# Optimization experiments

Measured on AMD Instinct MI355X. Metric: run time of the kernel, lower is better.

## Reference

```python
import jax, jax.numpy as jnp
import numpy as np

B, T, C, H = 2, 2048, 2048, 16
HD = C // H  # head dim = 128
BASE = 10000.0


def _rope_tables(seq_len, d):
    p = jnp.arange(d // 2, dtype=jnp.float32)
    # faithful to source: exponent uses 2**p (power of two), not 2*p
    theta = jnp.power(BASE, -(2.0 ** p) / d)            # [d/2]
    pos = jnp.arange(1, seq_len + 1, dtype=jnp.float32)[:, None]  # 1-indexed positions
    c = pos * theta                                      # [T, d/2]
    ang = jnp.concatenate([c, c], axis=-1)               # [T, d]
    return jnp.cos(ang), jnp.sin(ang)


def _rope(x):
    # x: [B, H, T, d]
    d = x.shape[-1]
    cos, sin = _rope_tables(x.shape[-2], d)
    half = d // 2
    x_rot = jnp.concatenate([-x[..., half:], x[..., :half]], axis=-1)
    return x * cos + x_rot * sin


def setup_inputs() -> dict:
    key = jax.random.key(0)
    k1, k2, k3 = jax.random.split(key, 3)
    x = jax.random.normal(k1, (B, T, C), dtype=jnp.float32)
    Wqkv = jax.random.normal(k2, (3 * C, C), dtype=jnp.float32) * 0.02
    bqkv = jnp.zeros((3 * C,), dtype=jnp.float32)
    Wo = jax.random.normal(k3, (C, C), dtype=jnp.float32) * 0.02
    bo = jnp.zeros((C,), dtype=jnp.float32)
    return {"x": x, "Wqkv": Wqkv, "bqkv": bqkv, "Wo": Wo, "bo": bo}


def reference(x, Wqkv, bqkv, Wo, bo):
    b, t, c = x.shape
    qkv = x @ Wqkv.T + bqkv                      # [B, T, 3C]
    q, k, v = jnp.split(qkv, 3, axis=-1)
    # [B, T, C] -> [B, H, T, HD]
    def to_heads(z):
        return z.reshape(b, t, H, HD).transpose(0, 2, 1, 3)
    q, k, v = to_heads(q), to_heads(k), to_heads(v)
    q = _rope(q)
    k = _rope(k)
    scale = 1.0 / jnp.sqrt(jnp.float32(HD))
    att = jnp.einsum('bhqd,bhkd->bhqk', q, k) * scale   # [B, H, T, T]
    causal = jnp.tril(jnp.ones((t, t), dtype=bool))
    att = jnp.where(causal, att, -jnp.inf)
    att = jax.nn.softmax(att, axis=-1)
    y = jnp.einsum('bhqk,bhkd->bhqd', att, v)           # [B, H, T, HD]
    y = y.transpose(0, 2, 1, 3).reshape(b, t, c)
    y = y @ Wo.T + bo
    return y
```

## Files before the change

kernel.cpp:

```cpp
#include <hip/hip_runtime.h>
#include <hip/hip_bf16.h>


typedef __attribute__((ext_vector_type(8))) short short8;
typedef __attribute__((ext_vector_type(4))) float f32x4;

#define B_  2
#define T_  2048
#define C_  2048
#define H_  16
#define HD_ 128

#define BARRIER() asm volatile("s_barrier" ::: "memory")
#define LGKM0()   asm volatile("s_waitcnt lgkmcnt(0)" ::: "memory")

template<int N> __device__ __forceinline__ void vmwait() {
  if constexpr (N == 8)      asm volatile("s_waitcnt vmcnt(8)" ::: "memory");
  else if constexpr (N == 6) asm volatile("s_waitcnt vmcnt(6)" ::: "memory");
  else if constexpr (N == 4) asm volatile("s_waitcnt vmcnt(4)" ::: "memory");
  else if constexpr (N == 3) asm volatile("s_waitcnt vmcnt(3)" ::: "memory");
  else if constexpr (N == 0) asm volatile("s_waitcnt vmcnt(0)" ::: "memory");
}

__device__ __forceinline__ float bf2f(unsigned short u) {
  union { unsigned int i; float f; } v; v.i = ((unsigned int)u) << 16; return v.f;
}
__device__ __forceinline__ unsigned short f2bf(float f) {
  union { float f; unsigned int i; } v; v.f = f;
  unsigned int x = v.i;
  return (unsigned short)((x + 0x7fffu + ((x >> 16) & 1u)) >> 16);
}
__device__ __forceinline__ float fexp2(float x) {
#if __has_builtin(__builtin_amdgcn_exp2f)
  return __builtin_amdgcn_exp2f(x);
#else
  return exp2f(x);
#endif
}

__device__ __forceinline__ void gll16(const unsigned short* g, unsigned short* lds_base) {
  __builtin_amdgcn_global_load_lds(
      (const __attribute__((address_space(1))) void*)g,
      (__attribute__((address_space(3))) void*)lds_base, 16, 0, 0);
}

__global__ void cvt_k(const float* __restrict__ src, unsigned short* __restrict__ dst, int n4)
{
  int i = blockIdx.x * blockDim.x + threadIdx.x;
  if (i < n4) {
    float4 v = ((const float4*)src)[i];
    ushort4 h;
    h.x = f2bf(v.x); h.y = f2bf(v.y); h.z = f2bf(v.z); h.w = f2bf(v.w);
    ((ushort4*)dst)[i] = h;
  }
}

__device__ __forceinline__ void stage_unit(
    const unsigned short* __restrict__ G, int K, int t, int kk,
    unsigned short (&L)[2][2][2][256][32], int buf, int mat,
    int wave, int sra, int ca8)
{
  const unsigned short* s = G + (size_t)sra * K + t * 64 + kk * 32 + ca8;
  gll16(s,                   &L[buf][kk][mat][wave * 16][0]);
  gll16(s + (size_t)128 * K, &L[buf][kk][mat][128 + wave * 16][0]);
}

template<int CB, bool SN1, bool SN2, int V0, int V1, int V2, int V3>
__device__ __forceinline__ void ktile256(
    int t,
    const unsigned short* __restrict__ Ag,
    const unsigned short* __restrict__ Bg, int K,
    unsigned short (&L)[2][2][2][256][32],
    f32x4 (&acc)[8][4],
    int wave, int wm, int wn, int l15, int csw8, int sra, int ca8)
{
  short8 af[4], bf[4];

#pragma unroll
  for (int n = 0; n < 4; ++n)
    bf[n] = *(const short8*)&L[CB][0][1][wn * 64 + n * 16 + l15][csw8];
#pragma unroll
  for (int j = 0; j < 4; ++j)
    af[j] = *(const short8*)&L[CB][0][0][wm * 128 + j * 16 + l15][csw8];
  if constexpr (SN1)
    stage_unit(Ag, K, t + 1, 1, L, CB ^ 1, 0, wave, sra, ca8);
  BARRIER();
  LGKM0();
  __builtin_amdgcn_s_setprio(1);
#pragma unroll
  for (int j = 0; j < 4; ++j)
#pragma unroll
    for (int n = 0; n < 4; ++n)
      acc[j][n] = __builtin_amdgcn_mfma_f32_16x16x32_bf16(af[j], bf[n], acc[j][n], 0, 0, 0);
  __builtin_amdgcn_s_setprio(0);
  vmwait<V0>();
  BARRIER();

#pragma unroll
  for (int j = 0; j < 4; ++j)
    af[j] = *(const short8*)&L[CB][0][0][wm * 128 + 64 + j * 16 + l15][csw8];
  if constexpr (SN1)
    stage_unit(Bg, K, t + 1, 1, L, CB ^ 1, 1, wave, sra, ca8);
  BARRIER();
  LGKM0();
  __builtin_amdgcn_s_setprio(1);
#pragma unroll
  for (int j = 0; j < 4; ++j)
#pragma unroll
    for (int n = 0; n < 4; ++n)
      acc[4 + j][n] = __builtin_amdgcn_mfma_f32_16x16x32_bf16(af[j], bf[n], acc[4 + j][n], 0, 0, 0);
  __builtin_amdgcn_s_setprio(0);
  vmwait<V1>();
  BARRIER();

#pragma unroll
  for (int n = 0; n < 4; ++n)
    bf[n] = *(const short8*)&L[CB][1][1][wn * 64 + n * 16 + l15][csw8];
#pragma unroll
  for (int j = 0; j < 4; ++j)
    af[j] = *(const short8*)&L[CB][1][0][wm * 128 + j * 16 + l15][csw8];
  if constexpr (SN2)
    stage_unit(Ag, K, t + 2, 0, L, CB, 0, wave, sra, ca8);
  BARRIER();
  LGKM0();
  __builtin_amdgcn_s_setprio(1);
#pragma unroll
  for (int j = 0; j < 4; ++j)
#pragma unroll
    for (int n = 0; n < 4; ++n)
      acc[j][n] = __builtin_amdgcn_mfma_f32_16x16x32_bf16(af[j], bf[n], acc[j][n], 0, 0, 0);
  __builtin_amdgcn_s_setprio(0);
  vmwait<V2>();
  BARRIER();

#pragma unroll
  for (int j = 0; j < 4; ++j)
    af[j] = *(const short8*)&L[CB][1][0][wm * 128 + 64 + j * 16 + l15][csw8];
  if constexpr (SN2)
    stage_unit(Bg, K, t + 2, 0, L, CB, 1, wave, sra, ca8);
  BARRIER();
  LGKM0();
  __builtin_amdgcn_s_setprio(1);
#pragma unroll
  for (int j = 0; j < 4; ++j)
#pragma unroll
    for (int n = 0; n < 4; ++n)
      acc[4 + j][n] = __builtin_amdgcn_mfma_f32_16x16x32_bf16(af[j], bf[n], acc[4 + j][n], 0, 0, 0);
  __builtin_amdgcn_s_setprio(0);
  vmwait<V3>();
  BARRIER();
}

template<int MODE>
__global__ __launch_bounds__(512, 2)
void gemm256(const unsigned short* __restrict__ A,
             const unsigned short* __restrict__ Bw,
             const float* __restrict__ bias,
             float* __restrict__ Cout,
             unsigned short* __restrict__ Qb,
             unsigned short* __restrict__ Kb,
             unsigned short* __restrict__ Vb,
             int N, int K)
{
  __shared__ unsigned short L[2][2][2][256][32];

  const int tid  = threadIdx.x;
  const int wave = tid >> 6, lane = tid & 63;
  const int quad = lane >> 4, l15 = lane & 15;
  const int wm = wave >> 2, wn = wave & 3;
  const int csw8 = (quad ^ ((l15 >> 1) & 3)) * 8;
  const int sra = tid >> 2;
  const int ca8 = ((tid & 3) ^ ((sra >> 1) & 3)) * 8;

  const int n0 = blockIdx.x * 256;
  const int m0 = blockIdx.y * 256;
  const unsigned short* Ag = A  + (size_t)m0 * K;
  const unsigned short* Bg = Bw + (size_t)n0 * K;

  f32x4 acc[8][4];
#pragma unroll
  for (int i = 0; i < 8; i++)
#pragma unroll
    for (int j = 0; j < 4; j++) acc[i][j] = (f32x4){0.f, 0.f, 0.f, 0.f};

  stage_unit(Ag, K, 0, 0, L, 0, 0, wave, sra, ca8);
  stage_unit(Bg, K, 0, 0, L, 0, 1, wave, sra, ca8);
  stage_unit(Ag, K, 0, 1, L, 0, 0, wave, sra, ca8);
  stage_unit(Bg, K, 0, 1, L, 0, 1, wave, sra, ca8);
  stage_unit(Ag, K, 1, 0, L, 1, 0, wave, sra, ca8);
  stage_unit(Bg, K, 1, 0, L, 1, 1, wave, sra, ca8);
  vmwait<8>();
  BARRIER();

  const int NT = K >> 6;
#pragma unroll 1
  for (int t = 0; t + 3 < NT; t += 2) {
    ktile256<0, true, true, 8, 8, 8, 8>(t,     Ag, Bg, K, L, acc, wave, wm, wn, l15, csw8, sra, ca8);
    ktile256<1, true, true, 8, 8, 8, 8>(t + 1, Ag, Bg, K, L, acc, wave, wm, wn, l15, csw8, sra, ca8);
  }
  ktile256<0, true,  false, 8,  8,  8,  4>(NT - 2, Ag, Bg, K, L, acc, wave, wm, wn, l15, csw8, sra, ca8);
  ktile256<1, false, false, -1, 0, -1, -1>(NT - 1, Ag, Bg, K, L, acc, wave, wm, wn, l15, csw8, sra, ca8);

  if constexpr (MODE == 0) {
#pragma unroll
    for (int mi = 0; mi < 8; mi++)
#pragma unroll
      for (int n = 0; n < 4; n++) {
        int col = n0 + wn * 64 + n * 16 + l15;
        float bv = bias[col];
#pragma unroll
        for (int r = 0; r < 4; r++) {
          int row = m0 + wm * 128 + mi * 16 + quad * 4 + r;
          Cout[(size_t)row * N + col] = acc[mi][n][r] + bv;
        }
      }
  } else {
    const int which = n0 >> 11;
    unsigned short* P = (which == 0) ? Qb : (which == 1) ? Kb : Vb;
#pragma unroll
    for (int mi = 0; mi < 8; mi++)
#pragma unroll
      for (int n = 0; n < 4; n++) {
        int col = n0 + wn * 64 + n * 16 + l15;
        float bv = bias[col];
        int h = (col >> 7) & 15, d = col & 127;
#pragma unroll
        for (int r = 0; r < 4; r++) {
          int m = m0 + wm * 128 + mi * 16 + quad * 4 + r;
          int b = m >> 11, t = m & (T_ - 1);
          size_t addr = (which == 2)
              ? ((size_t)((b * H_ + h) * HD_ + d)) * T_ + t
              : ((size_t)((b * H_ + h) * T_ + t)) * HD_ + d;
          P[addr] = f2bf(acc[mi][n][r] + bv);
        }
      }
  }
}

__global__ void rope_k(unsigned short* __restrict__ Q, unsigned short* __restrict__ K)
{
  const int tid = threadIdx.x;
  const int w = tid >> 6, l = tid & 63;
  const int r = blockIdx.x * 4 + w;
  const int t = r & (T_ - 1);
  const float pos = (float)(t + 1);
  const float theta = expf(-exp2f((float)l) * 0.07195578415606394f);
  const float ang = pos * theta;
  const float c = cosf(ang), s = sinf(ang);
  const float QS = 0.08838834764831845f * 1.4426950408889634f;
  const size_t base = (size_t)r * HD_;

  float q0 = bf2f(Q[base + l]), q1 = bf2f(Q[base + l + 64]);
  Q[base + l]      = f2bf((q0 * c - q1 * s) * QS);
  Q[base + l + 64] = f2bf((q1 * c + q0 * s) * QS);
  float k0 = bf2f(K[base + l]), k1 = bf2f(K[base + l + 64]);
  K[base + l]      = f2bf(k0 * c - k1 * s);
  K[base + l + 64] = f2bf(k1 * c + k0 * s);
}

__global__ __launch_bounds__(256, 2)
void attn_k(const unsigned short* __restrict__ Q,
            const unsigned short* __restrict__ K,
            const unsigned short* __restrict__ Vt_g,
            unsigned short* __restrict__ AO)
{
  __shared__ unsigned short Kl[64 * 128];
  __shared__ unsigned short Vl[128 * 64];
  __shared__ unsigned short Pl[4 * 16 * 72];

  const int tid  = threadIdx.x;
  const int wave = tid >> 6, lane = tid & 63;
  const int quad = lane >> 4, l15 = lane & 15;
  const int blk = blockIdx.x;
  const int bh = (blk & 7) + 8 * ((blk >> 3) & 3);
  const int qp = (blk >> 5) & 15;
  const unsigned short* Qh = Q    + (size_t)bh * T_ * HD_;
  const unsigned short* Kh = K    + (size_t)bh * T_ * HD_;
  const unsigned short* Vh = Vt_g + (size_t)bh * T_ * HD_;
  const int b = bh >> 4, h = bh & 15;

#pragma unroll
  for (int tile = 0; tile < 2; tile++) {
    const int q0 = (tile == 0 ? qp : 31 - qp) * 64;
    const int wq = q0 + wave * 16;
    short8 qf[4];
#pragma unroll
    for (int kc = 0; kc < 4; kc++)
      qf[kc] = *(const short8*)&Qh[(size_t)(wq + l15) * HD_ + kc * 32 + quad * 8];

    f32x4 oacc[8];
#pragma unroll
    for (int n = 0; n < 8; n++) oacc[n] = (f32x4){0.f, 0.f, 0.f, 0.f};
    float mst[4], lst[4];
#pragma unroll
    for (int r = 0; r < 4; r++) { mst[r] = -1e30f; lst[r] = 0.f; }

    const int niter = (q0 >> 6) + 1;
    for (int it = 0; it < niter; it++) {
      const int kt = it * 64;
      __syncthreads();
#pragma unroll
      for (int i = 0; i < 4; i++) {
        int cc = i * 256 + wave * 64 + lane;
        int kr = cc >> 4, kcs = (cc & 15) ^ (kr & 15);
        gll16(Kh + (size_t)(kt + kr) * HD_ + kcs * 8, &Kl[(i * 4 + wave) * 512]);
        int vr = cc >> 3, vcs = (cc & 7) ^ (vr & 7);
        gll16(Vh + (size_t)vr * T_ + kt + vcs * 8, &Vl[(i * 4 + wave) * 512]);
      }
      __syncthreads();

      f32x4 sa[4];
#pragma unroll
      for (int ni = 0; ni < 4; ni++) sa[ni] = (f32x4){0.f, 0.f, 0.f, 0.f};
#pragma unroll
      for (int kc = 0; kc < 4; kc++) {
        const int cswK = (((kc * 4 + quad) ^ l15) * 8);
        short8 bfr[4];
#pragma unroll
        for (int ni = 0; ni < 4; ni++)
          bfr[ni] = *(const short8*)&Kl[(ni * 16 + l15) * HD_ + cswK];
#pragma unroll
        for (int ni = 0; ni < 4; ni++)
          sa[ni] = __builtin_amdgcn_mfma_f32_16x16x32_bf16(qf[kc], bfr[ni], sa[ni], 0, 0, 0);
      }

      if (kt == q0) {
#pragma unroll
        for (int ni = 0; ni < 4; ni++) {
          int gcol = kt + ni * 16 + l15;
#pragma unroll
          for (int r = 0; r < 4; r++) {
            int grow = wq + quad * 4 + r;
            if (gcol > grow) sa[ni][r] = -1e30f;
          }
        }
      }

      float rmax[4] = {-1e30f, -1e30f, -1e30f, -1e30f};
#pragma unroll
      for (int ni = 0; ni < 4; ni++)
#pragma unroll
        for (int r = 0; r < 4; r++) rmax[r] = fmaxf(rmax[r], sa[ni][r]);
#pragma unroll
      for (int r = 0; r < 4; r++)
#pragma unroll
        for (int off = 1; off < 16; off <<= 1)
          rmax[r] = fmaxf(rmax[r], __shfl_xor(rmax[r], off));
      float alpha[4];
#pragma unroll
      for (int r = 0; r < 4; r++) {
        float mnew = fmaxf(mst[r], rmax[r]);
        alpha[r] = fexp2(fminf(mst[r] - mnew, 0.f));
        mst[r] = mnew;
      }
      float rsum[4] = {0.f, 0.f, 0.f, 0.f};
#pragma unroll
      for (int ni = 0; ni < 4; ni++)
#pragma unroll
        for (int r = 0; r < 4; r++) {
          float p = fexp2(fminf(sa[ni][r] - mst[r], 0.f));
          sa[ni][r] = p;
          rsum[r] += p;
        }
#pragma unroll
      for (int r = 0; r < 4; r++) {
#pragma unroll
        for (int off = 1; off < 16; off <<= 1)
          rsum[r] += __shfl_xor(rsum[r], off);
        lst[r] = lst[r] * alpha[r] + rsum[r];
      }
#pragma unroll
      for (int nv = 0; nv < 8; nv++)
#pragma unroll
        for (int r = 0; r < 4; r++) oacc[nv][r] *= alpha[r];
#pragma unroll
      for (int ni = 0; ni < 4; ni++)
#pragma unroll
        for (int r = 0; r < 4; r++)
          Pl[wave * 16 * 72 + (quad * 4 + r) * 72 + ni * 16 + l15] = f2bf(sa[ni][r]);
      __syncthreads();

      short8 pf[2];
#pragma unroll
      for (int kc = 0; kc < 2; kc++)
        pf[kc] = *(const short8*)&Pl[wave * 16 * 72 + l15 * 72 + kc * 32 + quad * 8];
#pragma unroll
      for (int kc = 0; kc < 2; kc++) {
        const int cswV = (((kc * 4 + quad) ^ (l15 & 7)) * 8);
#pragma unroll
        for (int nv = 0; nv < 8; nv++) {
          short8 vb = *(const short8*)&Vl[(nv * 16 + l15) * 64 + cswV];
          oacc[nv] = __builtin_amdgcn_mfma_f32_16x16x32_bf16(pf[kc], vb, oacc[nv], 0, 0, 0);
        }
      }
    }

    float linv[4];
#pragma unroll
    for (int r = 0; r < 4; r++) linv[r] = 1.0f / fmaxf(lst[r], 1e-20f);
#pragma unroll
    for (int nv = 0; nv < 8; nv++)
#pragma unroll
      for (int r = 0; r < 4; r++) {
        int t = wq + quad * 4 + r;
        int d = nv * 16 + l15;
        AO[((size_t)(b * T_ + t)) * C_ + h * HD_ + d] = f2bf(oacc[nv][r] * linv[r]);
      }
  }
}

template<int A32, int B32, int MODE>
__global__ __launch_bounds__(256, 2)
void gemm_nt(const void* __restrict__ Ap, const void* __restrict__ Bp,
             const float* __restrict__ bias,
             float* __restrict__ Cout,
             unsigned short* __restrict__ Qb,
             unsigned short* __restrict__ Kb,
             unsigned short* __restrict__ Vb,
             int N, int K)
{
  __shared__ unsigned short Al[128 * 72];
  __shared__ unsigned short Bl[128 * 72];
  const int tid  = threadIdx.x;
  const int wave = tid >> 6, lane = tid & 63;
  const int quad = lane >> 4, l15 = lane & 15;
  const int wm = wave >> 1, wn = wave & 1;
  const int n0 = blockIdx.x * 128, m0 = blockIdx.y * 128;

  f32x4 acc[4][4];
#pragma unroll
  for (int i = 0; i < 4; i++)
#pragma unroll
    for (int j = 0; j < 4; j++) acc[i][j] = (f32x4){0.f, 0.f, 0.f, 0.f};

  for (int k0 = 0; k0 < K; k0 += 64) {
    __syncthreads();
    if constexpr (A32) {
      const float* A = (const float*)Ap;
#pragma unroll
      for (int i = 0; i < 8; i++) {
        int cid = tid + i * 256;
        int r = cid >> 4, c = cid & 15;
        float4 v = *(const float4*)&A[(size_t)(m0 + r) * K + k0 + c * 4];
        ushort4 hh;
        hh.x = f2bf(v.x); hh.y = f2bf(v.y); hh.z = f2bf(v.z); hh.w = f2bf(v.w);
        *(ushort4*)&Al[r * 72 + c * 4] = hh;
      }
    } else {
      const unsigned short* A = (const unsigned short*)Ap;
#pragma unroll
      for (int i = 0; i < 4; i++) {
        int cid = tid + i * 256;
        int r = cid >> 3, c = cid & 7;
        *(float4*)&Al[r * 72 + c * 8] =
            *(const float4*)&A[(size_t)(m0 + r) * K + k0 + c * 8];
      }
    }
    if constexpr (B32) {
      const float* Bm = (const float*)Bp;
#pragma unroll
      for (int i = 0; i < 8; i++) {
        int cid = tid + i * 256;
        int r = cid >> 4, c = cid & 15;
        float4 v = *(const float4*)&Bm[(size_t)(n0 + r) * K + k0 + c * 4];
        ushort4 hh;
        hh.x = f2bf(v.x); hh.y = f2bf(v.y); hh.z = f2bf(v.z); hh.w = f2bf(v.w);
        *(ushort4*)&Bl[r * 72 + c * 4] = hh;
      }
    } else {
      const unsigned short* Bm = (const unsigned short*)Bp;
#pragma unroll
      for (int i = 0; i < 4; i++) {
        int cid = tid + i * 256;
        int r = cid >> 3, c = cid & 7;
        *(float4*)&Bl[r * 72 + c * 8] =
            *(const float4*)&Bm[(size_t)(n0 + r) * K + k0 + c * 8];
      }
    }
    __syncthreads();
#pragma unroll
    for (int kc = 0; kc < 2; kc++) {
      short8 af[4], bfr[4];
#pragma unroll
      for (int mi = 0; mi < 4; mi++)
        af[mi] = *(const short8*)&Al[(wm * 64 + mi * 16 + l15) * 72 + kc * 32 + quad * 8];
#pragma unroll
      for (int ni = 0; ni < 4; ni++)
        bfr[ni] = *(const short8*)&Bl[(wn * 64 + ni * 16 + l15) * 72 + kc * 32 + quad * 8];
#pragma unroll
      for (int mi = 0; mi < 4; mi++)
#pragma unroll
        for (int ni = 0; ni < 4; ni++)
          acc[mi][ni] = __builtin_amdgcn_mfma_f32_16x16x32_bf16(af[mi], bfr[ni], acc[mi][ni], 0, 0, 0);
    }
  }

  if constexpr (MODE == 0) {
#pragma unroll
    for (int mi = 0; mi < 4; mi++)
#pragma unroll
      for (int ni = 0; ni < 4; ni++) {
        int col = n0 + wn * 64 + ni * 16 + l15;
        float bv = bias[col];
#pragma unroll
        for (int r = 0; r < 4; r++) {
          int row = m0 + wm * 64 + mi * 16 + quad * 4 + r;
          Cout[(size_t)row * N + col] = acc[mi][ni][r] + bv;
        }
      }
  } else {
    int which = n0 >> 11;
    int h = (n0 >> 7) & 15;
    unsigned short* P = (which == 0) ? Qb : (which == 1) ? Kb : Vb;
#pragma unroll
    for (int mi = 0; mi < 4; mi++)
#pragma unroll
      for (int ni = 0; ni < 4; ni++) {
        int d = wn * 64 + ni * 16 + l15;
        float bv = bias[n0 + d];
#pragma unroll
        for (int r = 0; r < 4; r++) {
          int m = m0 + wm * 64 + mi * 16 + quad * 4 + r;
          int b = m >> 11, t = m & (T_ - 1);
          size_t addr = (which == 2)
              ? ((size_t)((b * H_ + h) * HD_ + d)) * T_ + t
              : ((size_t)((b * H_ + h) * T_ + t)) * HD_ + d;
          P[addr] = f2bf(acc[mi][ni][r] + bv);
        }
      }
  }
}

extern "C" void kernel_launch(void* const* d_in, const int* in_sizes, int n_in,
                              void* d_out, int out_size, void* d_ws, size_t ws_size,
                              hipStream_t stream)
{
  const float* x    = (const float*)d_in[0];
  const float* Wqkv = (const float*)d_in[1];
  const float* bqkv = (const float*)d_in[2];
  const float* Wo   = (const float*)d_in[3];
  const float* bo   = (const float*)d_in[4];
  float* out = (float*)d_out;

  const size_t SZ   = (size_t)B_ * H_ * T_ * HD_;
  const size_t NX   = SZ;
  const size_t NWQ  = (size_t)3 * C_ * C_;
  const size_t NWO  = (size_t)C_ * C_;
  unsigned short* ws = (unsigned short*)d_ws;

  dim3 blk(256, 1, 1);
  dim3 blk512(512, 1, 1);
  const size_t need = (NX + NWQ + 3 * SZ) * sizeof(unsigned short);

  if (ws_size >= need) {
    unsigned short* xb    = ws;
    unsigned short* Wqkvb = xb + NX;
    unsigned short* Qb    = Wqkvb + NWQ;
    unsigned short* Kb    = Qb + SZ;
    unsigned short* Vb    = Kb + SZ;
    unsigned short* AO    = xb;
    unsigned short* Wob   = Wqkvb;

    cvt_k<<<dim3((unsigned)(NX / 1024)), blk, 0, stream>>>(x, xb, (int)(NX / 4));
    cvt_k<<<dim3((unsigned)(NWQ / 1024)), blk, 0, stream>>>(Wqkv, Wqkvb, (int)(NWQ / 4));
    gemm256<1><<<dim3(24, 16, 1), blk512, 0, stream>>>(
        xb, Wqkvb, bqkv, nullptr, Qb, Kb, Vb, 6144, 2048);
    cvt_k<<<dim3((unsigned)(NWO / 1024)), blk, 0, stream>>>(Wo, Wob, (int)(NWO / 4));
    rope_k<<<dim3((B_ * H_ * T_) / 4, 1, 1), blk, 0, stream>>>(Qb, Kb);
    attn_k<<<dim3(512, 1, 1), blk, 0, stream>>>(Qb, Kb, Vb, AO);
    gemm256<0><<<dim3(8, 16, 1), blk512, 0, stream>>>(
        AO, Wob, bo, out, nullptr, nullptr, nullptr, 2048, 2048);
  } else {
    unsigned short* Qb = ws;
    unsigned short* Kb = Qb + SZ;
    unsigned short* Vb = Kb + SZ;
    unsigned short* AO = Vb + SZ;
    gemm_nt<1, 1, 1><<<dim3(48, 32, 1), blk, 0, stream>>>(
        (const void*)x, (const void*)Wqkv, bqkv, nullptr, Qb, Kb, Vb, 6144, 2048);
    rope_k<<<dim3((B_ * H_ * T_) / 4, 1, 1), blk, 0, stream>>>(Qb, Kb);
    attn_k<<<dim3(512, 1, 1), blk, 0, stream>>>(Qb, Kb, Vb, AO);
    gemm_nt<0, 1, 0><<<dim3(16, 32, 1), blk, 0, stream>>>(
        (const void*)AO, (const void*)Wo, bo, out, nullptr, nullptr, nullptr, 2048, 2048);
  }
}
```

Measured before the change: 432.4 us.

## Double-buffer GEMM LDS fragments in registers to overlap reads with MFMA

Restructures the 256x256 GEMM k-tile loop so A/B fragments are held in two register sets. Each phase's LDS reads now prefetch operands for a later MFMA phase, including the next tile's first fragments, instead of being read and then waited on with lgkmcnt(0) right before use. The vmcnt waits are rebalanced and two of the four per-tile global-load waits are removed. This aims to hide LDS latency behind MFMA work, at the cost of more live VGPRs and less explicit LDS wait ordering.

```diff
diff --git a/kernel.cpp b/kernel.cpp
--- a/kernel.cpp
+++ b/kernel.cpp
@@ -12,13 +12,11 @@
 #define HD_ 128
 
 #define BARRIER() asm volatile("s_barrier" ::: "memory")
-#define LGKM0()   asm volatile("s_waitcnt lgkmcnt(0)" ::: "memory")
 
 template<int N> __device__ __forceinline__ void vmwait() {
   if constexpr (N == 8)      asm volatile("s_waitcnt vmcnt(8)" ::: "memory");
   else if constexpr (N == 6) asm volatile("s_waitcnt vmcnt(6)" ::: "memory");
   else if constexpr (N == 4) asm volatile("s_waitcnt vmcnt(4)" ::: "memory");
-  else if constexpr (N == 3) asm volatile("s_waitcnt vmcnt(3)" ::: "memory");
   else if constexpr (N == 0) asm volatile("s_waitcnt vmcnt(0)" ::: "memory");
 }
 
@@ -65,89 +63,85 @@
   gll16(s + (size_t)128 * K, &L[buf][kk][mat][128 + wave * 16][0]);
 }
 
-template<int CB, bool SN1, bool SN2, int V0, int V1, int V2, int V3>
+template<int CB, bool SN1, bool SN2, int V0, int V2, bool RD3>
 __device__ __forceinline__ void ktile256(
     int t,
     const unsigned short* __restrict__ Ag,
     const unsigned short* __restrict__ Bg, int K,
     unsigned short (&L)[2][2][2][256][32],
     f32x4 (&acc)[8][4],
+    short8 (&af0)[4], short8 (&af1)[4],
+    short8 (&bf0)[4], short8 (&bf1)[4],
     int wave, int wm, int wn, int l15, int csw8, int sra, int ca8)
 {
-  short8 af[4], bf[4];
-
-#pragma unroll
-  for (int n = 0; n < 4; ++n)
-    bf[n] = *(const short8*)&L[CB][0][1][wn * 64 + n * 16 + l15][csw8];
-#pragma unroll
-  for (int j = 0; j < 4; ++j)
-    af[j] = *(const short8*)&L[CB][0][0][wm * 128 + j * 16 + l15][csw8];
+#pragma unroll
+  for (int j = 0; j < 4; ++j)
+    af1[j] = *(const short8*)&L[CB][0][0][wm * 128 + 64 + j * 16 + l15][csw8];
   if constexpr (SN1)
     stage_unit(Ag, K, t + 1, 1, L, CB ^ 1, 0, wave, sra, ca8);
   BARRIER();
-  LGKM0();
   __builtin_amdgcn_s_setprio(1);
 #pragma unroll
   for (int j = 0; j < 4; ++j)
 #pragma unroll
     for (int n = 0; n < 4; ++n)
-      acc[j][n] = __builtin_amdgcn_mfma_f32_16x16x32_bf16(af[j], bf[n], acc[j][n], 0, 0, 0);
+      acc[j][n] = __builtin_amdgcn_mfma_f32_16x16x32_bf16(af0[j], bf0[n], acc[j][n], 0, 0, 0);
   __builtin_amdgcn_s_setprio(0);
   vmwait<V0>();
   BARRIER();
 
 #pragma unroll
-  for (int j = 0; j < 4; ++j)
-    af[j] = *(const short8*)&L[CB][0][0][wm * 128 + 64 + j * 16 + l15][csw8];
+  for (int n = 0; n < 4; ++n)
+    bf1[n] = *(const short8*)&L[CB][1][1][wn * 64 + n * 16 + l15][csw8];
+#pragma unroll
+  for (int j = 0; j < 4; ++j)
+    af0[j] = *(const short8*)&L[CB][1][0][wm * 128 + j * 16 + l15][csw8];
   if constexpr (SN1)
     stage_unit(Bg, K, t + 1, 1, L, CB ^ 1, 1, wave, sra, ca8);
   BARRIER();
-  LGKM0();
   __builtin_amdgcn_s_setprio(1);
 #pragma unroll
   for (int j = 0; j < 4; ++j)
 #pragma unroll
     for (int n = 0; n < 4; ++n)
-      acc[4 + j][n] = __builtin_amdgcn_mfma_f32_16x16x32_bf16(af[j], bf[n], acc[4 + j][n], 0, 0, 0);
+      acc[4 + j][n] = __builtin_amdgcn_mfma_f32_16x16x32_bf16(af1[j], bf0[n], acc[4 + j][n], 0, 0, 0);
   __builtin_amdgcn_s_setprio(0);
-  vmwait<V1>();
-  BARRIER();
-
-#pragma unroll
-  for (int n = 0; n < 4; ++n)
-    bf[n] = *(const short8*)&L[CB][1][1][wn * 64 + n * 16 + l15][csw8];
-#pragma unroll
-  for (int j = 0; j < 4; ++j)
-    af[j] = *(const short8*)&L[CB][1][0][wm * 128 + j * 16 + l15][csw8];
+  BARRIER();
+
+#pragma unroll
+  for (int j = 0; j < 4; ++j)
+    af1[j] = *(const short8*)&L[CB][1][0][wm * 128 + 64 + j * 16 + l15][csw8];
   if constexpr (SN2)
     stage_unit(Ag, K, t + 2, 0, L, CB, 0, wave, sra, ca8);
   BARRIER();
-  LGKM0();
   __builtin_amdgcn_s_setprio(1);
 #pragma unroll
   for (int j = 0; j < 4; ++j)
 #pragma unroll
     for (int n = 0; n < 4; ++n)
-      acc[j][n] = __builtin_amdgcn_mfma_f32_16x16x32_bf16(af[j], bf[n], acc[j][n], 0, 0, 0);
+      acc[j][n] = __builtin_amdgcn_mfma_f32_16x16x32_bf16(af0[j], bf1[n], acc[j][n], 0, 0, 0);
   __builtin_amdgcn_s_setprio(0);
   vmwait<V2>();
   BARRIER();
 
-#pragma unroll
-  for (int j = 0; j < 4; ++j)
-    af[j] = *(const short8*)&L[CB][1][0][wm * 128 + 64 + j * 16 + l15][csw8];
+  if constexpr (RD3) {
+#pragma unroll
+    for (int n = 0; n < 4; ++n)
+      bf0[n] = *(const short8*)&L[CB ^ 1][0][1][wn * 64 + n * 16 + l15][csw8];
+#pragma unroll
+    for (int j = 0; j < 4; ++j)
+      af0[j] = *(const short8*)&L[CB ^ 1][0][0][wm * 128 + j * 16 + l15][csw8];
+  }
   if constexpr (SN2)
     stage_unit(Bg, K, t + 2, 0, L, CB, 1, wave, sra, ca8);
   BARRIER();
-  LGKM0();
   __builtin_amdgcn_s_setprio(1);
 #pragma unroll
   for (int j = 0; j < 4; ++j)
 #pragma unroll
     for (int n = 0; n < 4; ++n)
-      acc[4 + j][n] = __builtin_amdgcn_mfma_f32_16x16x32_bf16(af[j], bf[n], acc[4 + j][n], 0, 0, 0);
+      acc[4 + j][n] = __builtin_amdgcn_mfma_f32_16x16x32_bf16(af1[j], bf1[n], acc[4 + j][n], 0, 0, 0);
   __builtin_amdgcn_s_setprio(0);
-  vmwait<V3>();
   BARRIER();
 }
 
@@ -183,6 +177,8 @@
 #pragma unroll
     for (int j = 0; j < 4; j++) acc[i][j] = (f32x4){0.f, 0.f, 0.f, 0.f};
 
+  short8 af0[4], af1[4], bf0[4], bf1[4];
+
   stage_unit(Ag, K, 0, 0, L, 0, 0, wave, sra, ca8);
   stage_unit(Bg, K, 0, 0, L, 0, 1, wave, sra, ca8);
   stage_unit(Ag, K, 0, 1, L, 0, 0, wave, sra, ca8);
@@ -191,15 +187,21 @@
   stage_unit(Bg, K, 1, 0, L, 1, 1, wave, sra, ca8);
   vmwait<8>();
   BARRIER();
+#pragma unroll
+  for (int n = 0; n < 4; ++n)
+    bf0[n] = *(const short8*)&L[0][0][1][wn * 64 + n * 16 + l15][csw8];
+#pragma unroll
+  for (int j = 0; j < 4; ++j)
+    af0[j] = *(const short8*)&L[0][0][0][wm * 128 + j * 16 + l15][csw8];
 
   const int NT = K >> 6;
 #pragma unroll 1
   for (int t = 0; t + 3 < NT; t += 2) {
-    ktile256<0, true, true, 8, 8, 8, 8>(t,     Ag, Bg, K, L, acc, wave, wm, wn, l15, csw8, sra, ca8);
-    ktile256<1, true, true, 8, 8, 8, 8>(t + 1, Ag, Bg, K, L, acc, wave, wm, wn, l15, csw8, sra, ca8);
-  }
-  ktile256<0, true,  false, 8,  8,  8,  4>(NT - 2, Ag, Bg, K, L, acc, wave, wm, wn, l15, csw8, sra, ca8);
-  ktile256<1, false, false, -1, 0, -1, -1>(NT - 1, Ag, Bg, K, L, acc, wave, wm, wn, l15, csw8, sra, ca8);
+    ktile256<0, true, true, 6, 6, true>(t,     Ag, Bg, K, L, acc, af0, af1, bf0, bf1, wave, wm, wn, l15, csw8, sra, ca8);
+    ktile256<1, true, true, 6, 6, true>(t + 1, Ag, Bg, K, L, acc, af0, af1, bf0, bf1, wave, wm, wn, l15, csw8, sra, ca8);
+  }
+  ktile256<0, true,  false, 6,  4, true >(NT - 2, Ag, Bg, K, L, acc, af0, af1, bf0, bf1, wave, wm, wn, l15, csw8, sra, ca8);
+  ktile256<1, false, false, 0, -1, false>(NT - 1, Ag, Bg, K, L, acc, af0, af1, bf0, bf1, wave, wm, wn, l15, csw8, sra, ca8);
 
   if constexpr (MODE == 0) {
 #pragma unroll
```

After: 420.6 us. 2.7% less time.
